# Kernel tuning notes

Hardware: AMD Instinct MI355X
Metric: run time of the kernel (lower is better)

The kernel has to match this reference:

```python
import jax, jax.numpy as jnp
import numpy as np

B, C, H, W = 16, 64, 64, 64
HEADS = 8

def conv1x1(x, w):
    # x: [B, Cin, H, W], w: [Cout, Cin] -> [B, Cout, H, W]
    return jnp.einsum('oc,bchw->bohw', w, x)

def maxpool2x2(x):
    b, c, h, w = x.shape
    return x.reshape(b, c, h // 2, 2, w // 2, 2).max(axis=(3, 5))

def setup_inputs() -> dict:
    key = jax.random.key(0)
    ks = jax.random.split(key, 6)
    x = jax.random.normal(ks[0], (B, C, H, W), dtype=jnp.float32)
    w_theta = jax.random.normal(ks[1], (C // HEADS, C), dtype=jnp.float32) * 0.05
    w_phi = jax.random.normal(ks[2], (C // HEADS, C), dtype=jnp.float32) * 0.05
    w_g = jax.random.normal(ks[3], (C // 2, C), dtype=jnp.float32) * 0.05
    w_o = jax.random.normal(ks[4], (C, C // 2), dtype=jnp.float32) * 0.05
    gamma = jax.random.normal(ks[5], (), dtype=jnp.float32)
    return {'x': x, 'w_theta': w_theta, 'w_phi': w_phi, 'w_g': w_g, 'w_o': w_o, 'gamma': gamma}

def reference(x, w_theta, w_phi, w_g, w_o, gamma):
    b, c, h, w = x.shape
    n = h * w                      # query length
    m = n // 4                     # kv length after 2x2 maxpool
    theta = conv1x1(x, w_theta).reshape(b, c // HEADS, n)   # [B, C/h, N]
    phi = maxpool2x2(conv1x1(x, w_phi)).reshape(b, c // HEADS, m)  # [B, C/h, M]
    g = maxpool2x2(conv1x1(x, w_g)).reshape(b, c // 2, m)   # [B, C/2, M]
    # attention: theta^T @ phi -> [B, N, M]; NOTE: no 1/sqrt(d) scaling (SAGAN)
    beta = jax.nn.softmax(jnp.einsum('bdn,bdm->bnm', theta, phi), axis=-1)
    # o = g @ beta^T -> [B, C/2, N]
    o = jnp.einsum('bdm,bnm->bdn', g, beta).reshape(b, c // 2, h, w)
    o = conv1x1(o, w_o)            # [B, C, H, W]
    return gamma * o + x
```

## Files before the change

### kernel.cpp

```cpp
#include <hip/hip_runtime.h>
#include <hip/hip_bf16.h>

#define NB 16
#define NC 64
#define NN 4096
#define NM 1024
#define ND 8
#define NG 32

typedef short short8 __attribute__((ext_vector_type(8)));
typedef float floatx4 __attribute__((ext_vector_type(4)));

#define LOG2E 1.44269504f

__device__ __forceinline__ short f2bfs(float f) {
    union { __hip_bfloat16 h; short s; } u;
    u.h = __float2bfloat16(f);
    return u.s;
}
__device__ __forceinline__ unsigned pack2bf(float a, float b) {
    return (unsigned)(unsigned short)f2bfs(a) | ((unsigned)(unsigned short)f2bfs(b) << 16);
}
__device__ __forceinline__ unsigned pk2fast(float a, float b) {
    unsigned ua = __float_as_uint(a) + 0x8000u;
    unsigned ub = __float_as_uint(b) + 0x8000u;
    return __builtin_amdgcn_perm(ub, ua, 0x07060302);
}
__device__ __forceinline__ short8 u4s8(uint4 v) {
    union { uint4 u; short8 s; } c; c.u = v; return c.s;
}

__global__ __launch_bounds__(256)
void proj_kernel(const float* __restrict__ x,
                 const float* __restrict__ w_theta,
                 const float* __restrict__ w_phi,
                 const float* __restrict__ w_g,
                 const float* __restrict__ w_o,
                 unsigned* __restrict__ theta_ws,
                 unsigned* __restrict__ phi_ws,
                 unsigned* __restrict__ g2_ws)
{
    __shared__ __align__(16) float xl[64 * 128];
    __shared__ float lwt[512];
    __shared__ float lwp[512];
    __shared__ float lwg[2048];
    __shared__ float lwo[2048];
    __shared__ __align__(16) float lgs[32 * 36];
    __shared__ float lps[32 * 8];

    const int b  = blockIdx.x >> 5;
    const int ph = blockIdx.x & 31;
    const int t  = threadIdx.x;

    for (int i = t; i < 512;  i += 256) { lwt[i] = w_theta[i]; lwp[i] = w_phi[i]; }
    for (int i = t; i < 2048; i += 256) { lwg[i] = w_g[i];     lwo[i] = w_o[i]; }

    const float* xb = x + (size_t)b * NC * NN + (size_t)ph * 128;
    for (int idx = t; idx < 2048; idx += 256) {
        int c = idx >> 5, i4 = idx & 31;
        ((float4*)xl)[c * 32 + i4] = ((const float4*)(xb + (size_t)c * NN))[i4];
    }
    __syncthreads();

    if (t < 128) {
        float th[8];
        #pragma unroll
        for (int oc = 0; oc < 8; ++oc) th[oc] = 0.f;
        for (int c = 0; c < 64; ++c) {
            float xv = xl[c * 128 + t];
            #pragma unroll
            for (int oc = 0; oc < 8; ++oc) th[oc] = fmaf(lwt[oc * 64 + c], xv, th[oc]);
        }
        uint4 pk;
        pk.x = pack2bf(th[0] * LOG2E, th[1] * LOG2E);
        pk.y = pack2bf(th[2] * LOG2E, th[3] * LOG2E);
        pk.z = pack2bf(th[4] * LOG2E, th[5] * LOG2E);
        pk.w = pack2bf(th[6] * LOG2E, th[7] * LOG2E);
        ((uint4*)theta_ws)[(size_t)b * NN + ph * 128 + t] = pk;

        int m = t >> 2, oc0 = (t & 3) * 2;
        float s[2][4];
        #pragma unroll
        for (int a = 0; a < 2; ++a)
            #pragma unroll
            for (int p = 0; p < 4; ++p) s[a][p] = 0.f;
        #pragma unroll 4
        for (int c = 0; c < 64; ++c) {
            const float* xr = &xl[c * 128];
            float x0 = xr[2 * m], x1 = xr[2 * m + 1], x2 = xr[64 + 2 * m], x3 = xr[65 + 2 * m];
            #pragma unroll
            for (int a = 0; a < 2; ++a) {
                float w = lwp[(oc0 + a) * 64 + c];
                s[a][0] = fmaf(w, x0, s[a][0]);
                s[a][1] = fmaf(w, x1, s[a][1]);
                s[a][2] = fmaf(w, x2, s[a][2]);
                s[a][3] = fmaf(w, x3, s[a][3]);
            }
        }
        #pragma unroll
        for (int a = 0; a < 2; ++a)
            lps[m * 8 + oc0 + a] = fmaxf(fmaxf(s[a][0], s[a][1]), fmaxf(s[a][2], s[a][3]));
    } else {
        int tt = t - 128;
        int oc0 = (tt >> 3) * 2, grp = tt & 7;
        float s0[16], s1[16];
        #pragma unroll
        for (int i = 0; i < 16; ++i) { s0[i] = 0.f; s1[i] = 0.f; }
        const float4* xl4 = (const float4*)xl;
        #pragma unroll 2
        for (int c = 0; c < 64; ++c) {
            float4 a0 = xl4[c * 32 + 2 * grp];
            float4 a1 = xl4[c * 32 + 2 * grp + 1];
            float4 b0 = xl4[c * 32 + 16 + 2 * grp];
            float4 b1 = xl4[c * 32 + 17 + 2 * grp];
            float w0 = lwg[oc0 * 64 + c], w1 = lwg[(oc0 + 1) * 64 + c];
            s0[0] = fmaf(w0, a0.x, s0[0]);  s0[1] = fmaf(w0, a0.y, s0[1]);
            s0[2] = fmaf(w0, a0.z, s0[2]);  s0[3] = fmaf(w0, a0.w, s0[3]);
            s0[4] = fmaf(w0, a1.x, s0[4]);  s0[5] = fmaf(w0, a1.y, s0[5]);
            s0[6] = fmaf(w0, a1.z, s0[6]);  s0[7] = fmaf(w0, a1.w, s0[7]);
            s0[8] = fmaf(w0, b0.x, s0[8]);  s0[9] = fmaf(w0, b0.y, s0[9]);
            s0[10] = fmaf(w0, b0.z, s0[10]); s0[11] = fmaf(w0, b0.w, s0[11]);
            s0[12] = fmaf(w0, b1.x, s0[12]); s0[13] = fmaf(w0, b1.y, s0[13]);
            s0[14] = fmaf(w0, b1.z, s0[14]); s0[15] = fmaf(w0, b1.w, s0[15]);
            s1[0] = fmaf(w1, a0.x, s1[0]);  s1[1] = fmaf(w1, a0.y, s1[1]);
            s1[2] = fmaf(w1, a0.z, s1[2]);  s1[3] = fmaf(w1, a0.w, s1[3]);
            s1[4] = fmaf(w1, a1.x, s1[4]);  s1[5] = fmaf(w1, a1.y, s1[5]);
            s1[6] = fmaf(w1, a1.z, s1[6]);  s1[7] = fmaf(w1, a1.w, s1[7]);
            s1[8] = fmaf(w1, b0.x, s1[8]);  s1[9] = fmaf(w1, b0.y, s1[9]);
            s1[10] = fmaf(w1, b0.z, s1[10]); s1[11] = fmaf(w1, b0.w, s1[11]);
            s1[12] = fmaf(w1, b1.x, s1[12]); s1[13] = fmaf(w1, b1.y, s1[13]);
            s1[14] = fmaf(w1, b1.z, s1[14]); s1[15] = fmaf(w1, b1.w, s1[15]);
        }
        #pragma unroll
        for (int p = 0; p < 4; ++p) {
            float v0 = fmaxf(fmaxf(s0[2 * p], s0[2 * p + 1]), fmaxf(s0[8 + 2 * p], s0[9 + 2 * p]));
            float v1 = fmaxf(fmaxf(s1[2 * p], s1[2 * p + 1]), fmaxf(s1[8 + 2 * p], s1[9 + 2 * p]));
            lgs[oc0 * 36 + grp * 4 + p]       = v0;
            lgs[(oc0 + 1) * 36 + grp * 4 + p] = v1;
        }
    }
    __syncthreads();

    {
        int co = t >> 2, sel = t & 3;
        int m0a = 4 * sel, m0b = 16 + 4 * sel;
        float v[8];
        #pragma unroll
        for (int mm = 0; mm < 8; ++mm) v[mm] = 0.f;
        #pragma unroll 4
        for (int c = 0; c < 32; ++c) {
            float w = lwo[co * 32 + c];
            float4 ga = *(const float4*)&lgs[c * 36 + m0a];
            float4 gb = *(const float4*)&lgs[c * 36 + m0b];
            v[0] = fmaf(w, ga.x, v[0]); v[1] = fmaf(w, ga.y, v[1]);
            v[2] = fmaf(w, ga.z, v[2]); v[3] = fmaf(w, ga.w, v[3]);
            v[4] = fmaf(w, gb.x, v[4]); v[5] = fmaf(w, gb.y, v[5]);
            v[6] = fmaf(w, gb.z, v[6]); v[7] = fmaf(w, gb.w, v[7]);
        }
        uint4 pk;
        pk.x = pack2bf(v[0], v[1]); pk.y = pack2bf(v[2], v[3]);
        pk.z = pack2bf(v[4], v[5]); pk.w = pack2bf(v[6], v[7]);
        int lane = (sel << 4) | (co & 15);
        ((uint4*)g2_ws)[(((size_t)b * 4 + (co >> 4)) * 32 + ph) * 64 + lane] = pk;
    }

    if (t < 32) {
        const float* pr = &lps[t * 8];
        uint4 pk;
        pk.x = pack2bf(pr[0], pr[1]); pk.y = pack2bf(pr[2], pr[3]);
        pk.z = pack2bf(pr[4], pr[5]); pk.w = pack2bf(pr[6], pr[7]);
        ((uint4*)phi_ws)[(size_t)b * NM + ph * 32 + t] = pk;
    }
}

__global__ __launch_bounds__(256, 2)
void attn_kernel(const unsigned* __restrict__ theta_ws,
                 const unsigned* __restrict__ phi_ws,
                 const unsigned* __restrict__ g2_ws,
                 const float* __restrict__ gamma_p,
                 const float* __restrict__ x,
                 float* __restrict__ out)
{
    __shared__ __align__(16) uint4 lphi[NM];

    const int b    = blockIdx.x >> 5;
    const int qblk = blockIdx.x & 31;
    const int t    = threadIdx.x;
    const int w    = t >> 6;
    const int lane = t & 63;
    const int lm   = lane & 15;
    const int quad = lane >> 4;
    const int q0   = qblk * 128 + w * 32;

    for (int kk = t; kk < NM; kk += 256)
        lphi[kk] = ((const uint4*)phi_ws)[(size_t)b * NM + kk];

    uint4 tb[2];
    #pragma unroll
    for (int qt = 0; qt < 2; ++qt) {
        uint4 v = ((const uint4*)theta_ws)[(size_t)b * NN + q0 + qt * 16 + lm];
        tb[qt].x = quad == 0 ? v.x : 0u;
        tb[qt].y = quad == 0 ? v.y : 0u;
        tb[qt].z = quad == 0 ? v.z : 0u;
        tb[qt].w = quad == 0 ? v.w : 0u;
    }

    floatx4 acc[2][4];
    #pragma unroll
    for (int qt = 0; qt < 2; ++qt)
        #pragma unroll
        for (int ct = 0; ct < 4; ++ct) acc[qt][ct] = (floatx4)0.f;
    float lsum[2] = {0.f, 0.f};

    const uint4* gf = (const uint4*)g2_ws;
    uint4 ga[4], gn[4];
    #pragma unroll
    for (int ct = 0; ct < 4; ++ct)
        ga[ct] = gf[(((size_t)b * 4 + ct) * 32 + 0) * 64 + lane];

    __syncthreads();

    uint4 pp0 = lphi[lm];
    uint4 pp1 = lphi[16 + lm];

    for (int kg = 0; kg < 32; ++kg) {
        if (kg + 1 < 32) {
            #pragma unroll
            for (int ct = 0; ct < 4; ++ct)
                gn[ct] = gf[(((size_t)b * 4 + ct) * 32 + kg + 1) * 64 + lane];
        }
        uint4 pn0, pn1;
        if (kg + 1 < 32) {
            pn0 = lphi[(kg + 1) * 32 + lm];
            pn1 = lphi[(kg + 1) * 32 + 16 + lm];
        }

        #pragma unroll
        for (int qt = 0; qt < 2; ++qt) {
            floatx4 s0 = __builtin_amdgcn_mfma_f32_16x16x32_bf16(
                u4s8(pp0), u4s8(tb[qt]), (floatx4)0.f, 0, 0, 0);
            floatx4 s1 = __builtin_amdgcn_mfma_f32_16x16x32_bf16(
                u4s8(pp1), u4s8(tb[qt]), (floatx4)0.f, 0, 0, 0);
            float e0[4], e1[4];
            #pragma unroll
            for (int r = 0; r < 4; ++r) { e0[r] = exp2f(s0[r]); e1[r] = exp2f(s1[r]); }
            lsum[qt] += ((e0[0] + e0[1]) + (e0[2] + e0[3]))
                      + ((e1[0] + e1[1]) + (e1[2] + e1[3]));
            uint4 pb0 = make_uint4(pk2fast(e0[0], e0[1]), pk2fast(e0[2], e0[3]), 0u, 0u);
            uint4 pb1 = make_uint4(pk2fast(e1[0], e1[1]), pk2fast(e1[2], e1[3]), 0u, 0u);
            #pragma unroll
            for (int ct = 0; ct < 4; ++ct) {
                acc[qt][ct] = __builtin_amdgcn_mfma_f32_16x16x32_bf16(
                    u4s8(ga[ct]), u4s8(pb0), acc[qt][ct], 0, 0, 0);
                uint4 a1 = make_uint4(ga[ct].z, ga[ct].w, ga[ct].z, ga[ct].w);
                acc[qt][ct] = __builtin_amdgcn_mfma_f32_16x16x32_bf16(
                    u4s8(a1), u4s8(pb1), acc[qt][ct], 0, 0, 0);
            }
        }
        #pragma unroll
        for (int ct = 0; ct < 4; ++ct) ga[ct] = gn[ct];
        pp0 = pn0; pp1 = pn1;
    }

    float inv[2];
    {
        float l0 = lsum[0]; l0 += __shfl_xor(l0, 16); l0 += __shfl_xor(l0, 32);
        float l1 = lsum[1]; l1 += __shfl_xor(l1, 16); l1 += __shfl_xor(l1, 32);
        inv[0] = 1.0f / l0; inv[1] = 1.0f / l1;
    }

    const float gamma = gamma_p[0];
    #pragma unroll
    for (int qt = 0; qt < 2; ++qt) {
        const int q = q0 + qt * 16 + lm;
        #pragma unroll
        for (int ct = 0; ct < 4; ++ct) {
            #pragma unroll
            for (int r = 0; r < 4; ++r) {
                int co = ct * 16 + quad * 4 + r;
                size_t idx = ((size_t)b * NC + co) * NN + q;
                out[idx] = fmaf(gamma, acc[qt][ct][r] * inv[qt], x[idx]);
            }
        }
    }
}

extern "C" void kernel_launch(void* const* d_in, const int* in_sizes, int n_in,
                              void* d_out, int out_size, void* d_ws, size_t ws_size,
                              hipStream_t stream)
{
    const float* x  = (const float*)d_in[0];
    const float* wt = (const float*)d_in[1];
    const float* wp = (const float*)d_in[2];
    const float* wg = (const float*)d_in[3];
    const float* wo = (const float*)d_in[4];
    const float* gm = (const float*)d_in[5];
    float* out = (float*)d_out;

    unsigned* theta_ws = (unsigned*)d_ws;
    unsigned* phi_ws   = theta_ws + (size_t)NB * NN * ND / 2;
    unsigned* g2_ws    = phi_ws   + (size_t)NB * NM * ND / 2;

    proj_kernel<<<NB * 32, 256, 0, stream>>>(x, wt, wp, wg, wo, theta_ws, phi_ws, g2_ws);
    attn_kernel<<<NB * 32, 256, 0, stream>>>(theta_ws, phi_ws, g2_ws, gm, x, out);
}
```

Baseline: 121.2 us.

## Halve attention query tile, merge PV MFMAs, coalesce epilogue via LDS, transpose proj weights

The attention kernel now gives each wave 16 queries instead of 32, which doubles the grid to 1024 blocks and raises launch bounds to 4 blocks per CU for more parallelism and occupancy. The two half-K PV MFMAs are merged into one full-K MFMA by packing both exp tiles into a single operand. The output epilogue is staged through LDS so x is read and out is written as coalesced float4, and exp2f is swapped for the hardware intrinsic. In the projection kernel, w_g and w_o are stored transposed and padded in LDS to avoid bank conflicts. The trade-off is that the g2 and phi loads are repeated across twice as many blocks.

```diff
diff --git a/kernel.cpp b/kernel.cpp
--- a/kernel.cpp
+++ b/kernel.cpp
@@ -43,8 +43,8 @@
     __shared__ __align__(16) float xl[64 * 128];
     __shared__ float lwt[512];
     __shared__ float lwp[512];
-    __shared__ float lwg[2048];
-    __shared__ float lwo[2048];
+    __shared__ __align__(8) float lwgT[64 * 34];
+    __shared__ float lwoT[32 * 65];
     __shared__ __align__(16) float lgs[32 * 36];
     __shared__ float lps[32 * 8];
 
@@ -53,7 +53,10 @@
     const int t  = threadIdx.x;
 
     for (int i = t; i < 512;  i += 256) { lwt[i] = w_theta[i]; lwp[i] = w_phi[i]; }
-    for (int i = t; i < 2048; i += 256) { lwg[i] = w_g[i];     lwo[i] = w_o[i]; }
+    for (int i = t; i < 2048; i += 256) {
+        lwgT[(i & 63) * 34 + (i >> 6)] = w_g[i];
+        lwoT[(i & 31) * 65 + (i >> 5)] = w_o[i];
+    }
 
     const float* xb = x + (size_t)b * NC * NN + (size_t)ph * 128;
     for (int idx = t; idx < 2048; idx += 256) {
@@ -113,7 +116,8 @@
             float4 a1 = xl4[c * 32 + 2 * grp + 1];
             float4 b0 = xl4[c * 32 + 16 + 2 * grp];
             float4 b1 = xl4[c * 32 + 17 + 2 * grp];
-            float w0 = lwg[oc0 * 64 + c], w1 = lwg[(oc0 + 1) * 64 + c];
+            float2 wv = *(const float2*)&lwgT[c * 34 + oc0];
+            float w0 = wv.x, w1 = wv.y;
             s0[0] = fmaf(w0, a0.x, s0[0]);  s0[1] = fmaf(w0, a0.y, s0[1]);
             s0[2] = fmaf(w0, a0.z, s0[2]);  s0[3] = fmaf(w0, a0.w, s0[3]);
             s0[4] = fmaf(w0, a1.x, s0[4]);  s0[5] = fmaf(w0, a1.y, s0[5]);
@@ -149,7 +153,7 @@
         for (int mm = 0; mm < 8; ++mm) v[mm] = 0.f;
         #pragma unroll 4
         for (int c = 0; c < 32; ++c) {
-            float w = lwo[co * 32 + c];
+            float w = lwoT[c * 65 + co];
             float4 ga = *(const float4*)&lgs[c * 36 + m0a];
             float4 gb = *(const float4*)&lgs[c * 36 + m0b];
             v[0] = fmaf(w, ga.x, v[0]); v[1] = fmaf(w, ga.y, v[1]);
@@ -173,7 +177,7 @@
     }
 }
 
-__global__ __launch_bounds__(256, 2)
+__global__ __launch_bounds__(256, 4)
 void attn_kernel(const unsigned* __restrict__ theta_ws,
                  const unsigned* __restrict__ phi_ws,
                  const unsigned* __restrict__ g2_ws,
@@ -181,36 +185,35 @@
                  const float* __restrict__ x,
                  float* __restrict__ out)
 {
-    __shared__ __align__(16) uint4 lphi[NM];
-
-    const int b    = blockIdx.x >> 5;
-    const int qblk = blockIdx.x & 31;
+    __shared__ __align__(16) float smem_f[64 * 68];
+    uint4* lphi = (uint4*)smem_f;
+    float* ltr  = smem_f;
+
+    const int b    = blockIdx.x >> 6;
+    const int qblk = blockIdx.x & 63;
     const int t    = threadIdx.x;
     const int w    = t >> 6;
     const int lane = t & 63;
     const int lm   = lane & 15;
     const int quad = lane >> 4;
-    const int q0   = qblk * 128 + w * 32;
+    const int q0   = qblk * 64 + w * 16;
 
     for (int kk = t; kk < NM; kk += 256)
         lphi[kk] = ((const uint4*)phi_ws)[(size_t)b * NM + kk];
 
-    uint4 tb[2];
+    uint4 tb;
+    {
+        uint4 v = ((const uint4*)theta_ws)[(size_t)b * NN + q0 + lm];
+        tb.x = quad == 0 ? v.x : 0u;
+        tb.y = quad == 0 ? v.y : 0u;
+        tb.z = quad == 0 ? v.z : 0u;
+        tb.w = quad == 0 ? v.w : 0u;
+    }
+
+    floatx4 acc[4];
     #pragma unroll
-    for (int qt = 0; qt < 2; ++qt) {
-        uint4 v = ((const uint4*)theta_ws)[(size_t)b * NN + q0 + qt * 16 + lm];
-        tb[qt].x = quad == 0 ? v.x : 0u;
-        tb[qt].y = quad == 0 ? v.y : 0u;
-        tb[qt].z = quad == 0 ? v.z : 0u;
-        tb[qt].w = quad == 0 ? v.w : 0u;
-    }
-
-    floatx4 acc[2][4];
-    #pragma unroll
-    for (int qt = 0; qt < 2; ++qt)
-        #pragma unroll
-        for (int ct = 0; ct < 4; ++ct) acc[qt][ct] = (floatx4)0.f;
-    float lsum[2] = {0.f, 0.f};
+    for (int ct = 0; ct < 4; ++ct) acc[ct] = (floatx4)0.f;
+    float lsum = 0.f;
 
     const uint4* gf = (const uint4*)g2_ws;
     uint4 ga[4], gn[4];
@@ -224,63 +227,68 @@
     uint4 pp1 = lphi[16 + lm];
 
     for (int kg = 0; kg < 32; ++kg) {
-        if (kg + 1 < 32) {
-            #pragma unroll
-            for (int ct = 0; ct < 4; ++ct)
-                gn[ct] = gf[(((size_t)b * 4 + ct) * 32 + kg + 1) * 64 + lane];
-        }
         uint4 pn0, pn1;
         if (kg + 1 < 32) {
             pn0 = lphi[(kg + 1) * 32 + lm];
             pn1 = lphi[(kg + 1) * 32 + 16 + lm];
-        }
-
-        #pragma unroll
-        for (int qt = 0; qt < 2; ++qt) {
-            floatx4 s0 = __builtin_amdgcn_mfma_f32_16x16x32_bf16(
-                u4s8(pp0), u4s8(tb[qt]), (floatx4)0.f, 0, 0, 0);
-            floatx4 s1 = __builtin_amdgcn_mfma_f32_16x16x32_bf16(
-                u4s8(pp1), u4s8(tb[qt]), (floatx4)0.f, 0, 0, 0);
-            float e0[4], e1[4];
             #pragma unroll
-            for (int r = 0; r < 4; ++r) { e0[r] = exp2f(s0[r]); e1[r] = exp2f(s1[r]); }
-            lsum[qt] += ((e0[0] + e0[1]) + (e0[2] + e0[3]))
-                      + ((e1[0] + e1[1]) + (e1[2] + e1[3]));
-            uint4 pb0 = make_uint4(pk2fast(e0[0], e0[1]), pk2fast(e0[2], e0[3]), 0u, 0u);
-            uint4 pb1 = make_uint4(pk2fast(e1[0], e1[1]), pk2fast(e1[2], e1[3]), 0u, 0u);
-            #pragma unroll
-            for (int ct = 0; ct < 4; ++ct) {
-                acc[qt][ct] = __builtin_amdgcn_mfma_f32_16x16x32_bf16(
-                    u4s8(ga[ct]), u4s8(pb0), acc[qt][ct], 0, 0, 0);
-                uint4 a1 = make_uint4(ga[ct].z, ga[ct].w, ga[ct].z, ga[ct].w);
-                acc[qt][ct] = __builtin_amdgcn_mfma_f32_16x16x32_bf16(
-                    u4s8(a1), u4s8(pb1), acc[qt][ct], 0, 0, 0);
-            }
-        }
+            for (int ct = 0; ct < 4; ++ct)
+                gn[ct] = gf[(((size_t)b * 4 + ct) * 32 + kg + 1) * 64 + lane];
+        }
+
+        floatx4 s0 = __builtin_amdgcn_mfma_f32_16x16x32_bf16(
+            u4s8(pp0), u4s8(tb), (floatx4)0.f, 0, 0, 0);
+        floatx4 s1 = __builtin_amdgcn_mfma_f32_16x16x32_bf16(
+            u4s8(pp1), u4s8(tb), (floatx4)0.f, 0, 0, 0);
+        float e0[4], e1[4];
+        #pragma unroll
+        for (int r = 0; r < 4; ++r) {
+            e0[r] = __builtin_amdgcn_exp2f(s0[r]);
+            e1[r] = __builtin_amdgcn_exp2f(s1[r]);
+        }
+        lsum += ((e0[0] + e0[1]) + (e0[2] + e0[3]))
+              + ((e1[0] + e1[1]) + (e1[2] + e1[3]));
+        uint4 pb = make_uint4(pk2fast(e0[0], e0[1]), pk2fast(e0[2], e0[3]),
+                              pk2fast(e1[0], e1[1]), pk2fast(e1[2], e1[3]));
+        #pragma unroll
+        for (int ct = 0; ct < 4; ++ct)
+            acc[ct] = __builtin_amdgcn_mfma_f32_16x16x32_bf16(
+                u4s8(ga[ct]), u4s8(pb), acc[ct], 0, 0, 0);
+
         #pragma unroll
         for (int ct = 0; ct < 4; ++ct) ga[ct] = gn[ct];
         pp0 = pn0; pp1 = pn1;
     }
 
-    float inv[2];
+    float inv;
     {
-        float l0 = lsum[0]; l0 += __shfl_xor(l0, 16); l0 += __shfl_xor(l0, 32);
-        float l1 = lsum[1]; l1 += __shfl_xor(l1, 16); l1 += __shfl_xor(l1, 32);
-        inv[0] = 1.0f / l0; inv[1] = 1.0f / l1;
+        float l = lsum;
+        l += __shfl_xor(l, 16);
+        l += __shfl_xor(l, 32);
+        inv = 1.0f / l;
     }
 
     const float gamma = gamma_p[0];
+
+    __syncthreads();
     #pragma unroll
-    for (int qt = 0; qt < 2; ++qt) {
-        const int q = q0 + qt * 16 + lm;
-        #pragma unroll
-        for (int ct = 0; ct < 4; ++ct) {
-            #pragma unroll
-            for (int r = 0; r < 4; ++r) {
-                int co = ct * 16 + quad * 4 + r;
-                size_t idx = ((size_t)b * NC + co) * NN + q;
-                out[idx] = fmaf(gamma, acc[qt][ct][r] * inv[qt], x[idx]);
-            }
+    for (int ct = 0; ct < 4; ++ct)
+        #pragma unroll
+        for (int r = 0; r < 4; ++r)
+            ltr[(ct * 16 + quad * 4 + r) * 68 + w * 16 + lm] = acc[ct][r] * inv;
+    __syncthreads();
+
+    {
+        const int co = t >> 2, seg = (t & 3) * 16;
+        size_t base = ((size_t)b * NC + co) * NN + qblk * 64 + seg;
+        const float* tr = &ltr[co * 68 + seg];
+        #pragma unroll
+        for (int i = 0; i < 4; ++i) {
+            float4 tv = ((const float4*)tr)[i];
+            float4 xv = *(const float4*)(x + base + i * 4);
+            float4 ov = make_float4(fmaf(gamma, tv.x, xv.x), fmaf(gamma, tv.y, xv.y),
+                                    fmaf(gamma, tv.z, xv.z), fmaf(gamma, tv.w, xv.w));
+            *(float4*)(out + base + i * 4) = ov;
         }
     }
 }
@@ -302,5 +310,5 @@
     unsigned* g2_ws    = phi_ws   + (size_t)NB * NM * ND / 2;
 
     proj_kernel<<<NB * 32, 256, 0, stream>>>(x, wt, wp, wg, wo, theta_ws, phi_ws, g2_ws);
-    attn_kernel<<<NB * 32, 256, 0, stream>>>(theta_ws, phi_ws, g2_ws, gm, x, out);
-}
+    attn_kernel<<<NB * 64, 256, 0, stream>>>(theta_ws, phi_ws, g2_ws, gm, x, out);
+}
```

Measured after the change: 113.8 us. 6.1% less time.
